# Kernel optimization log

Measured on AMD Instinct MI355X. Metric: run time of the kernel, lower is better.

## Reference

```python
import jax, jax.numpy as jnp
import numpy as np

EPS = 1e-6

def _rmsnorm(x, scale):
    # RMSNorm over last axis (TPNorm pre-norm)
    var = jnp.mean(jnp.square(x), axis=-1, keepdims=True)
    return x * jax.lax.rsqrt(var + EPS) * scale


def setup_inputs() -> dict:
    key = jax.random.key(0)
    ks = jax.random.split(key, 6)
    B, S, D, H, Dh = 2, 2048, 1024, 16, 64
    x = jax.random.normal(ks[0], (B, S, D), dtype=jnp.float32)
    norm_scale = jnp.ones((D,), dtype=jnp.float32)
    # lecun_normal-like scaling: std = 1/sqrt(fan_in)
    wq = jax.random.normal(ks[1], (D, H, Dh), dtype=jnp.float32) / np.sqrt(D)
    wk = jax.random.normal(ks[2], (D, H, Dh), dtype=jnp.float32) / np.sqrt(D)
    wv = jax.random.normal(ks[3], (D, H, Dh), dtype=jnp.float32) / np.sqrt(D)
    w_out = jax.random.normal(ks[4], (H, Dh, D), dtype=jnp.float32) / np.sqrt(H * Dh)
    b_out = jnp.zeros((D,), dtype=jnp.float32)
    return {"x": x, "norm_scale": norm_scale, "wq": wq, "wk": wk, "wv": wv,
            "w_out": w_out, "b_out": b_out}


def reference(x, norm_scale, wq, wk, wv, w_out, b_out):
    dtype = x.dtype
    softmax_dtype = jnp.float32
    h = _rmsnorm(x, norm_scale)                                  # [B,S,D]
    q = jnp.einsum('bsd,dhe->bshe', h, wq)                       # [B,S,H,Dh]
    k = jnp.einsum('bsd,dhe->bshe', h, wk)
    v = jnp.einsum('bsd,dhe->bshe', h, wv)
    head_dim = q.shape[-1]
    scale = head_dim ** (-0.5)
    q = (q * scale).astype(softmax_dtype)
    kf = k.astype(softmax_dtype)
    weights = jnp.einsum('bqhd,bkhd->bhqk', q, kf)               # [B,H,S,S] fp32
    weights = jax.nn.softmax(weights, axis=-1).astype(dtype)
    new_vals = jnp.einsum('bhqk,bkhd->bqhd', weights, v).astype(dtype)
    out = jnp.einsum('bqhe,hed->bqd', new_vals, w_out) + b_out   # [B,S,D]
    return out
```

## Files before the change

### kernel.cpp

```cpp
#include <hip/hip_runtime.h>

typedef unsigned short u16;
typedef unsigned int   u32;
typedef __attribute__((ext_vector_type(8))) short bf16x8;
typedef __attribute__((ext_vector_type(4))) float f32x4;

#define SEQ 2048
#define DIM 1024
#define NH  16
#define DH  64
#define NROW 4096

static __device__ __forceinline__ float bf2f(u16 v){
  u32 u = ((u32)v) << 16; float f; __builtin_memcpy(&f, &u, 4); return f;
}
static __device__ __forceinline__ u16 f2bf(float f){
  u32 u; __builtin_memcpy(&u, &f, 4);
  u32 r = (u + 0x7fffu + ((u >> 16) & 1u)) >> 16;
  return (u16)r;
}
static __device__ __forceinline__ u32 pack2bf(float a, float b){
  u32 ua, ub; __builtin_memcpy(&ua, &a, 4); __builtin_memcpy(&ub, &b, 4);
  return ((ua + 0x8000u) >> 16) | ((ub + 0x8000u) & 0xFFFF0000u);
}
static __device__ __forceinline__ u32 cvt_pk_bf16(float a, float b){
  u32 r;
  asm("v_cvt_pk_bf16_f32 %0, %1, %2" : "=v"(r) : "v"(a), "v"(b));
  return r;
}

#define GLD_LDS(gp, lp) \
  __builtin_amdgcn_global_load_lds( \
      (const __attribute__((address_space(1))) void*)(gp), \
      (__attribute__((address_space(3))) void*)(lp), 16, 0, 0)

__global__ __launch_bounds__(256) void k_rmsnorm(const float* __restrict__ x,
                                                 const float* __restrict__ sc,
                                                 u16* __restrict__ h){
  int row = blockIdx.x, t = threadIdx.x;
  float4 v = ((const float4*)(x + (size_t)row * DIM))[t];
  float ss = v.x*v.x + v.y*v.y + v.z*v.z + v.w*v.w;
  #pragma unroll
  for (int d = 32; d; d >>= 1) ss += __shfl_down(ss, d, 64);
  __shared__ float red[4];
  if ((t & 63) == 0) red[t >> 6] = ss;
  __syncthreads();
  float tot = red[0] + red[1] + red[2] + red[3];
  float rms = rsqrtf(tot * (1.0f / DIM) + 1e-6f);
  float4 s4 = ((const float4*)sc)[t];
  u16 ov[4];
  ov[0] = f2bf(v.x * rms * s4.x);
  ov[1] = f2bf(v.y * rms * s4.y);
  ov[2] = f2bf(v.z * rms * s4.z);
  ov[3] = f2bf(v.w * rms * s4.w);
  ((uint2*)(h + (size_t)row * DIM))[t] = *(uint2*)ov;
}

__global__ __launch_bounds__(256) void k_wtrans(const float* __restrict__ in0,
                                                const float* __restrict__ in1,
                                                const float* __restrict__ in2,
                                                u16* __restrict__ outT){
  __shared__ u16 tile[64][68];
  int t = threadIdx.x;
  int c0 = blockIdx.x * 64;
  int r0 = blockIdx.y * 64;
  int z = blockIdx.z;
  const float* in = (z == 0) ? in0 : ((z == 1) ? in1 : in2);
  u16* out = outT + (size_t)z * (1u << 20);
  #pragma unroll
  for (int i = 0; i < 4; i++){
    int idx = t + 256 * i;
    int r = idx >> 4, c4 = (idx & 15) * 4;
    float4 v = *(const float4*)&in[(size_t)(r0 + r) * 1024 + c0 + c4];
    u16 pk[4] = {f2bf(v.x), f2bf(v.y), f2bf(v.z), f2bf(v.w)};
    *(uint2*)&tile[r][c4] = *(uint2*)pk;
  }
  __syncthreads();
  #pragma unroll
  for (int i = 0; i < 2; i++){
    int c = t + 256 * i;
    int n = c >> 3, koff = (c & 7) * 8;
    alignas(16) u16 vals[8];
    #pragma unroll
    for (int j = 0; j < 8; j++) vals[j] = tile[koff + j][n];
    *(uint4*)&out[(size_t)(c0 + n) * 1024 + r0 + koff] = *(uint4*)vals;
  }
}

__global__ __launch_bounds__(256) void k_gemm(const u16* __restrict__ A,
                                              const u16* __restrict__ B0,
                                              const u16* __restrict__ B1,
                                              const u16* __restrict__ B2,
                                              void* __restrict__ C0,
                                              void* __restrict__ C1,
                                              void* __restrict__ C2,
                                              const float* __restrict__ bias,
                                              int qkv){
  __shared__ u16 Al[128][32];
  __shared__ u16 Bl[128][32];
  int t = threadIdx.x, lane = t & 63, w = t >> 6;
  int wm = w & 1, wn = w >> 1;
  int mrow = lane & 15, quad = lane >> 4;
  int m0 = blockIdx.x * 128, n0 = blockIdx.y * 128;
  int z = blockIdx.z;
  const u16* Bt = (z == 0) ? B0 : ((z == 1) ? B1 : B2);

  int r0s = (t * 16) >> 6, off0 = ((t * 16) & 63) >> 1;
  int r1s = r0s + 64;

  f32x4 acc[4][4];
  #pragma unroll
  for (int ms = 0; ms < 4; ms++)
    #pragma unroll
    for (int ns = 0; ns < 4; ns++) acc[ms][ns] = (f32x4){0.f, 0.f, 0.f, 0.f};

  for (int kt = 0; kt < 32; kt++){
    int K0 = kt * 32;
    __syncthreads();
    GLD_LDS(&A [(size_t)(m0 + r0s) * 1024 + K0 + off0], &Al[r0s][off0]);
    GLD_LDS(&A [(size_t)(m0 + r1s) * 1024 + K0 + off0], &Al[r1s][off0]);
    GLD_LDS(&Bt[(size_t)(n0 + r0s) * 1024 + K0 + off0], &Bl[r0s][off0]);
    GLD_LDS(&Bt[(size_t)(n0 + r1s) * 1024 + K0 + off0], &Bl[r1s][off0]);
    __syncthreads();
    bf16x8 af[4], bf[4];
    #pragma unroll
    for (int ms = 0; ms < 4; ms++)
      af[ms] = *(const bf16x8*)&Al[wm * 64 + ms * 16 + mrow][quad * 8];
    #pragma unroll
    for (int ns = 0; ns < 4; ns++)
      bf[ns] = *(const bf16x8*)&Bl[wn * 64 + ns * 16 + mrow][quad * 8];
    #pragma unroll
    for (int ms = 0; ms < 4; ms++)
      #pragma unroll
      for (int ns = 0; ns < 4; ns++)
        acc[ms][ns] = __builtin_amdgcn_mfma_f32_16x16x32_bf16(af[ms], bf[ns], acc[ms][ns], 0, 0, 0);
  }

  float qscale = (qkv && z == 0) ? 0.180336880111112f : 1.0f;
  bool  vmode  = (qkv && z == 2);
  void* C = (z == 0) ? C0 : ((z == 1) ? C1 : C2);

  #pragma unroll
  for (int ms = 0; ms < 4; ms++){
    #pragma unroll
    for (int ns = 0; ns < 4; ns++){
      int col = n0 + wn * 64 + ns * 16 + mrow;
      int rbase = m0 + wm * 64 + ms * 16 + quad * 4;
      if (vmode){
        int b = rbase >> 11, sl = rbase & 2047;
        int hh = col >> 6, e = col & 63;
        uint2 pk = { pack2bf(acc[ms][ns][0], acc[ms][ns][1]),
                     pack2bf(acc[ms][ns][2], acc[ms][ns][3]) };
        *(uint2*)&((u16*)C)[(size_t)((b * NH + hh) * DH + e) * SEQ + sl] = pk;
      } else if (qkv){
        #pragma unroll
        for (int r = 0; r < 4; r++)
          ((u16*)C)[(size_t)(rbase + r) * 1024 + col] = f2bf(acc[ms][ns][r] * qscale);
      } else {
        float bv = bias ? bias[col] : 0.f;
        #pragma unroll
        for (int r = 0; r < 4; r++)
          ((float*)C)[(size_t)(rbase + r) * 1024 + col] = acc[ms][ns][r] + bv;
      }
    }
  }
}

__global__ __launch_bounds__(256) void k_attn(const u16* q,
                                              const u16* __restrict__ k,
                                              const u16* __restrict__ vt,
                                              u16* nv){
  __shared__ u16 Kl[2][64][64];
  __shared__ u16 Vl[2][64][64];
  int t = threadIdx.x, lane = t & 63, w = t >> 6;
  int mrow = lane & 15, quad = lane >> 4;
  int s0 = blockIdx.x * 64;
  int bh = blockIdx.y; int b = bh >> 4, hh = bh & 15;

  const u16* qrow = q + (size_t)((b * SEQ + s0 + w * 16 + mrow) * NH + hh) * DH;
  bf16x8 bq0 = *(const bf16x8*)(qrow + quad * 8);
  bf16x8 bq1 = *(const bf16x8*)(qrow + 32 + quad * 8);

  int rw  = t >> 3;
  int fst = (rw & 3) | (((t >> 6) & 1) << 2);
  int lc  = (t & 7) ^ fst;
  const u16* kp = k  + ((size_t)b * SEQ + rw) * (NH * DH) + hh * DH + lc * 8;
  const u16* vp = vt + ((size_t)bh * DH + rw) * SEQ + lc * 8;

  int row0 = ((mrow >> 2) << 3) | (mrow & 3);
  int cK = (quad ^ ((mrow & 3) | (((mrow >> 2) & 1) << 2))) << 4;
  int cV = (quad ^ ((mrow & 3) | (((mrow >> 3) & 1) << 2))) << 4;

  f32x4 o[4];
  #pragma unroll
  for (int g = 0; g < 4; g++) o[g] = (f32x4){0.f, 0.f, 0.f, 0.f};
  f32x4 accl = (f32x4){0.f, 0.f, 0.f, 0.f};
  bf16x8 onesf;
  #pragma unroll
  for (int j = 0; j < 8; j++) onesf[j] = (short)0x3F80;

  {
    u16* dK = &Kl[0][0][0]; u16* dV = &Vl[0][0][0];
    GLD_LDS(kp,                dK + (t << 3));
    GLD_LDS(kp + 32 * NH * DH, dK + ((t + 256) << 3));
    GLD_LDS(vp,                dV + (t << 3));
    GLD_LDS(vp + 32 * SEQ,     dV + ((t + 256) << 3));
    kp += 64 * NH * DH; vp += 64;
  }
  asm volatile("s_waitcnt vmcnt(0)" ::: "memory");
  __syncthreads();

  for (int kt = 0; kt < 32; kt++){
    int cur = kt & 1;
    if (kt < 31){
      u16* dK = &Kl[cur ^ 1][0][0]; u16* dV = &Vl[cur ^ 1][0][0];
      GLD_LDS(kp,                dK + (t << 3));
      GLD_LDS(kp + 32 * NH * DH, dK + ((t + 256) << 3));
      GLD_LDS(vp,                dV + (t << 3));
      GLD_LDS(vp + 32 * SEQ,     dV + ((t + 256) << 3));
      kp += 64 * NH * DH; vp += 64;
    }

    const char* Kb = (const char*)Kl[cur];
    f32x4 sT[4];
    #pragma unroll
    for (int g = 0; g < 4; g++){
      int rg = row0 + ((g & 1) << 2) + ((g >> 1) << 5);
      const char* rp = Kb + rg * 128;
      bf16x8 a0 = *(const bf16x8*)(rp + cK);
      bf16x8 a1 = *(const bf16x8*)(rp + (cK ^ 64));
      f32x4 zz = (f32x4){0.f, 0.f, 0.f, 0.f};
      zz = __builtin_amdgcn_mfma_f32_16x16x32_bf16(a0, bq0, zz, 0, 0, 0);
      zz = __builtin_amdgcn_mfma_f32_16x16x32_bf16(a1, bq1, zz, 0, 0, 0);
      sT[g] = zz;
    }

    u32 wd[8];
    #pragma unroll
    for (int g = 0; g < 4; g++){
      float e0 = exp2f(sT[g][0]), e1 = exp2f(sT[g][1]);
      float e2 = exp2f(sT[g][2]), e3 = exp2f(sT[g][3]);
      wd[g * 2]     = cvt_pk_bf16(e0, e1);
      wd[g * 2 + 1] = cvt_pk_bf16(e2, e3);
    }
    union { u32 u[4]; bf16x8 v; } U0, U1;
    U0.u[0] = wd[0]; U0.u[1] = wd[1]; U0.u[2] = wd[2]; U0.u[3] = wd[3];
    U1.u[0] = wd[4]; U1.u[1] = wd[5]; U1.u[2] = wd[6]; U1.u[3] = wd[7];
    bf16x8 pb0 = U0.v, pb1 = U1.v;

    accl = __builtin_amdgcn_mfma_f32_16x16x32_bf16(onesf, pb0, accl, 0, 0, 0);
    accl = __builtin_amdgcn_mfma_f32_16x16x32_bf16(onesf, pb1, accl, 0, 0, 0);

    const char* Vb = (const char*)Vl[cur];
    #pragma unroll
    for (int ge = 0; ge < 4; ge++){
      const char* rp = Vb + (ge * 16 + mrow) * 128;
      bf16x8 v0 = *(const bf16x8*)(rp + cV);
      bf16x8 v1 = *(const bf16x8*)(rp + (cV ^ 64));
      o[ge] = __builtin_amdgcn_mfma_f32_16x16x32_bf16(v0, pb0, o[ge], 0, 0, 0);
      o[ge] = __builtin_amdgcn_mfma_f32_16x16x32_bf16(v1, pb1, o[ge], 0, 0, 0);
    }

    asm volatile("s_waitcnt vmcnt(0)" ::: "memory");
    __syncthreads();
  }

  float rl = 1.0f / accl[0];
  u16* orow = nv + (size_t)((b * SEQ + s0 + w * 16 + mrow) * NH + hh) * DH;
  #pragma unroll
  for (int ge = 0; ge < 4; ge++){
    uint2 pk = { cvt_pk_bf16(o[ge][0] * rl, o[ge][1] * rl),
                 cvt_pk_bf16(o[ge][2] * rl, o[ge][3] * rl) };
    *(uint2*)&orow[ge * 16 + quad * 4] = pk;
  }
}

extern "C" void kernel_launch(void* const* d_in, const int* in_sizes, int n_in,
                              void* d_out, int out_size, void* d_ws, size_t ws_size,
                              hipStream_t stream){
  const float* x   = (const float*)d_in[0];
  const float* nsc = (const float*)d_in[1];
  const float* wq  = (const float*)d_in[2];
  const float* wk  = (const float*)d_in[3];
  const float* wv  = (const float*)d_in[4];
  const float* wo  = (const float*)d_in[5];
  const float* bo  = (const float*)d_in[6];
  char* ws = (char*)d_ws;
  const size_t MB = (size_t)1 << 20;

  u16* qb  = (u16*)(ws);
  u16* kb  = (u16*)(ws + 8  * MB);
  u16* vtb = (u16*)(ws + 16 * MB);
  u16* h   = (u16*)d_out;
  u16* wT  = (u16*)((char*)d_out + 8 * MB);
  u16* wqT = wT;
  u16* wkT = wT + (1u << 20);
  u16* wvT = wT + (2u << 20);
  u16* woT = kb;

  k_rmsnorm<<<NROW, 256, 0, stream>>>(x, nsc, h);
  k_wtrans<<<dim3(16, 16, 3), 256, 0, stream>>>(wq, wk, wv, wT);
  k_gemm<<<dim3(32, 8, 3), 256, 0, stream>>>(h, wqT, wkT, wvT, qb, kb, vtb, nullptr, 1);
  k_attn<<<dim3(32, 32, 1), 256, 0, stream>>>(qb, kb, vtb, qb);
  k_wtrans<<<dim3(16, 16, 1), 256, 0, stream>>>(wo, wo, wo, woT);
  k_gemm<<<dim3(32, 8, 1), 256, 0, stream>>>(qb, woT, woT, woT, d_out, d_out, d_out, bo, 0);
}
```

Before: 223.1 us.

## Double-buffer GEMM LDS tiles and widen attention blocks to 128 queries

The GEMM now double-buffers its A and B LDS tiles. It issues the next k-slice's global-to-LDS loads before computing on the current slice, which removes one barrier per iteration and overlaps memory with MFMA work. The attention kernel now launches 512-thread blocks covering 128 query rows, so each K/V tile loaded into LDS is shared by 8 waves instead of 4, and each thread issues half as many loads. The explicit vmcnt waits in attention are dropped, which relies on the barrier to order the asynchronous LDS loads. LDS use per GEMM block doubles, which may lower occupancy.

```diff
diff --git a/kernel.cpp b/kernel.cpp
--- a/kernel.cpp
+++ b/kernel.cpp
@@ -96,8 +96,8 @@
                                               void* __restrict__ C2,
                                               const float* __restrict__ bias,
                                               int qkv){
-  __shared__ u16 Al[128][32];
-  __shared__ u16 Bl[128][32];
+  __shared__ u16 Al[2][128][32];
+  __shared__ u16 Bl[2][128][32];
   int t = threadIdx.x, lane = t & 63, w = t >> 6;
   int wm = w & 1, wn = w >> 1;
   int mrow = lane & 15, quad = lane >> 4;
@@ -108,32 +108,45 @@
   int r0s = (t * 16) >> 6, off0 = ((t * 16) & 63) >> 1;
   int r1s = r0s + 64;
 
+  const u16* Ap0 = &A [(size_t)(m0 + r0s) * 1024 + off0];
+  const u16* Ap1 = &A [(size_t)(m0 + r1s) * 1024 + off0];
+  const u16* Bp0 = &Bt[(size_t)(n0 + r0s) * 1024 + off0];
+  const u16* Bp1 = &Bt[(size_t)(n0 + r1s) * 1024 + off0];
+
   f32x4 acc[4][4];
   #pragma unroll
   for (int ms = 0; ms < 4; ms++)
     #pragma unroll
     for (int ns = 0; ns < 4; ns++) acc[ms][ns] = (f32x4){0.f, 0.f, 0.f, 0.f};
 
+  GLD_LDS(Ap0, &Al[0][r0s][off0]);
+  GLD_LDS(Ap1, &Al[0][r1s][off0]);
+  GLD_LDS(Bp0, &Bl[0][r0s][off0]);
+  GLD_LDS(Bp1, &Bl[0][r1s][off0]);
+  __syncthreads();
+
   for (int kt = 0; kt < 32; kt++){
-    int K0 = kt * 32;
-    __syncthreads();
-    GLD_LDS(&A [(size_t)(m0 + r0s) * 1024 + K0 + off0], &Al[r0s][off0]);
-    GLD_LDS(&A [(size_t)(m0 + r1s) * 1024 + K0 + off0], &Al[r1s][off0]);
-    GLD_LDS(&Bt[(size_t)(n0 + r0s) * 1024 + K0 + off0], &Bl[r0s][off0]);
-    GLD_LDS(&Bt[(size_t)(n0 + r1s) * 1024 + K0 + off0], &Bl[r1s][off0]);
-    __syncthreads();
-    bf16x8 af[4], bf[4];
+    int cur = kt & 1;
+    if (kt < 31){
+      int K1 = (kt + 1) * 32;
+      GLD_LDS(Ap0 + K1, &Al[cur ^ 1][r0s][off0]);
+      GLD_LDS(Ap1 + K1, &Al[cur ^ 1][r1s][off0]);
+      GLD_LDS(Bp0 + K1, &Bl[cur ^ 1][r0s][off0]);
+      GLD_LDS(Bp1 + K1, &Bl[cur ^ 1][r1s][off0]);
+    }
+    bf16x8 af[4], bfr[4];
     #pragma unroll
     for (int ms = 0; ms < 4; ms++)
-      af[ms] = *(const bf16x8*)&Al[wm * 64 + ms * 16 + mrow][quad * 8];
+      af[ms] = *(const bf16x8*)&Al[cur][wm * 64 + ms * 16 + mrow][quad * 8];
     #pragma unroll
     for (int ns = 0; ns < 4; ns++)
-      bf[ns] = *(const bf16x8*)&Bl[wn * 64 + ns * 16 + mrow][quad * 8];
+      bfr[ns] = *(const bf16x8*)&Bl[cur][wn * 64 + ns * 16 + mrow][quad * 8];
     #pragma unroll
     for (int ms = 0; ms < 4; ms++)
       #pragma unroll
       for (int ns = 0; ns < 4; ns++)
-        acc[ms][ns] = __builtin_amdgcn_mfma_f32_16x16x32_bf16(af[ms], bf[ns], acc[ms][ns], 0, 0, 0);
+        acc[ms][ns] = __builtin_amdgcn_mfma_f32_16x16x32_bf16(af[ms], bfr[ns], acc[ms][ns], 0, 0, 0);
+    __syncthreads();
   }
 
   float qscale = (qkv && z == 0) ? 0.180336880111112f : 1.0f;
@@ -166,7 +179,7 @@
   }
 }
 
-__global__ __launch_bounds__(256) void k_attn(const u16* q,
+__global__ __launch_bounds__(512) void k_attn(const u16* q,
                                               const u16* __restrict__ k,
                                               const u16* __restrict__ vt,
                                               u16* nv){
@@ -174,7 +187,7 @@
   __shared__ u16 Vl[2][64][64];
   int t = threadIdx.x, lane = t & 63, w = t >> 6;
   int mrow = lane & 15, quad = lane >> 4;
-  int s0 = blockIdx.x * 64;
+  int s0 = blockIdx.x * 128;
   int bh = blockIdx.y; int b = bh >> 4, hh = bh & 15;
 
   const u16* qrow = q + (size_t)((b * SEQ + s0 + w * 16 + mrow) * NH + hh) * DH;
@@ -199,25 +212,16 @@
   #pragma unroll
   for (int j = 0; j < 8; j++) onesf[j] = (short)0x3F80;
 
-  {
-    u16* dK = &Kl[0][0][0]; u16* dV = &Vl[0][0][0];
-    GLD_LDS(kp,                dK + (t << 3));
-    GLD_LDS(kp + 32 * NH * DH, dK + ((t + 256) << 3));
-    GLD_LDS(vp,                dV + (t << 3));
-    GLD_LDS(vp + 32 * SEQ,     dV + ((t + 256) << 3));
-    kp += 64 * NH * DH; vp += 64;
-  }
-  asm volatile("s_waitcnt vmcnt(0)" ::: "memory");
+  GLD_LDS(kp, &Kl[0][0][0] + (t << 3));
+  GLD_LDS(vp, &Vl[0][0][0] + (t << 3));
+  kp += 64 * NH * DH; vp += 64;
   __syncthreads();
 
   for (int kt = 0; kt < 32; kt++){
     int cur = kt & 1;
     if (kt < 31){
-      u16* dK = &Kl[cur ^ 1][0][0]; u16* dV = &Vl[cur ^ 1][0][0];
-      GLD_LDS(kp,                dK + (t << 3));
-      GLD_LDS(kp + 32 * NH * DH, dK + ((t + 256) << 3));
-      GLD_LDS(vp,                dV + (t << 3));
-      GLD_LDS(vp + 32 * SEQ,     dV + ((t + 256) << 3));
+      GLD_LDS(kp, &Kl[cur ^ 1][0][0] + (t << 3));
+      GLD_LDS(vp, &Vl[cur ^ 1][0][0] + (t << 3));
       kp += 64 * NH * DH; vp += 64;
     }
 
@@ -261,7 +265,6 @@
       o[ge] = __builtin_amdgcn_mfma_f32_16x16x32_bf16(v1, pb1, o[ge], 0, 0, 0);
     }
 
-    asm volatile("s_waitcnt vmcnt(0)" ::: "memory");
     __syncthreads();
   }
 
@@ -301,7 +304,7 @@
   k_rmsnorm<<<NROW, 256, 0, stream>>>(x, nsc, h);
   k_wtrans<<<dim3(16, 16, 3), 256, 0, stream>>>(wq, wk, wv, wT);
   k_gemm<<<dim3(32, 8, 3), 256, 0, stream>>>(h, wqT, wkT, wvT, qb, kb, vtb, nullptr, 1);
-  k_attn<<<dim3(32, 32, 1), 256, 0, stream>>>(qb, kb, vtb, qb);
+  k_attn<<<dim3(16, 32, 1), 512, 0, stream>>>(qb, kb, vtb, qb);
   k_wtrans<<<dim3(16, 16, 1), 256, 0, stream>>>(wo, wo, wo, woT);
   k_gemm<<<dim3(32, 8, 1), 256, 0, stream>>>(qb, woT, woT, woT, d_out, d_out, d_out, bo, 0);
 }
```

Result: faster. 215.1 us (-3.6%).
